# Optimization experiments

Hardware: AMD Instinct MI355X
Metric: run time of the kernel (lower is better)

The kernel has to match this reference:

```python
import jax, jax.numpy as jnp
import numpy as np

N = 50000


def gcn_conv(x, W, b, src, dst, deg_inv_sqrt):
    # h = x @ W, then symmetric-normalized aggregation with self-loops
    h = x @ W  # [N, out]
    norm = deg_inv_sqrt[src] * deg_inv_sqrt[dst]  # [E]
    agg = jax.ops.segment_sum(h[src] * norm[:, None], dst, num_segments=N)
    # self-loop contribution: norm_ii = deg_inv_sqrt[i]^2
    agg = agg + h * (deg_inv_sqrt * deg_inv_sqrt)[:, None]
    return agg + b


def setup_inputs() -> dict:
    key = jax.random.key(0)
    ks = jax.random.split(key, 8)
    F_in, H, C = 128, 128, 64
    x = jax.random.normal(ks[0], (N, F_in), dtype=jnp.float32)
    edge_index = jax.random.randint(ks[1], (2, 800000), 0, N, dtype=jnp.int64)
    s = 1.0 / np.sqrt(F_in)
    W1 = jax.random.uniform(ks[2], (F_in, H), jnp.float32, -s, s)
    b1 = jnp.zeros((H,), jnp.float32)
    W2 = jax.random.uniform(ks[3], (H, H), jnp.float32, -s, s)
    b2 = jnp.zeros((H,), jnp.float32)
    W3 = jax.random.uniform(ks[4], (H, C), jnp.float32, -s, s)
    b3 = jnp.zeros((C,), jnp.float32)
    return {"x": x, "edge_index": edge_index, "W1": W1, "b1": b1,
            "W2": W2, "b2": b2, "W3": W3, "b3": b3}


def reference(x, edge_index, W1, b1, W2, b2, W3, b3):
    src, dst = edge_index[0], edge_index[1]
    # degree with self-loops (edge weight 1): deg[i] = in-degree + 1
    deg = jnp.zeros((N,), x.dtype).at[dst].add(1.0) + 1.0
    dinv = jax.lax.rsqrt(deg)
    h = gcn_conv(x, W1, b1, src, dst, dinv)
    h = jax.nn.relu(h)  # dropout p=0 / eval -> identity
    h = gcn_conv(h, W2, b2, src, dst, dinv)
    h = jax.nn.relu(h)
    h = gcn_conv(h, W3, b3, src, dst, dinv)
    return jax.nn.log_softmax(h, axis=-1)
```

## Files before the change

kernel.cpp:

```cpp
#include <hip/hip_runtime.h>
#include <math.h>

typedef short short8 __attribute__((ext_vector_type(8)));
typedef float floatx4 __attribute__((ext_vector_type(4)));

__device__ __forceinline__ float4 ld4(const float* p) { return *reinterpret_cast<const float4*>(p); }
__device__ __forceinline__ void st4(float* p, float4 v) { *reinterpret_cast<float4*>(p) = v; }

__device__ __forceinline__ float bf2f(unsigned int u) { return __uint_as_float(u << 16); }
__device__ __forceinline__ unsigned int f2bf1(float f) {
    unsigned int x = __float_as_uint(f);
    return (x + 0x7fffu + ((x >> 16) & 1u)) >> 16;
}
__device__ __forceinline__ unsigned int f2bf2(float lo, float hi) {
    return f2bf1(lo) | (f2bf1(hi) << 16);
}
__device__ __forceinline__ void unpack8(uint4 v, float* f) {
    f[0] = bf2f(v.x & 0xffffu); f[1] = bf2f(v.x >> 16);
    f[2] = bf2f(v.y & 0xffffu); f[3] = bf2f(v.y >> 16);
    f[4] = bf2f(v.z & 0xffffu); f[5] = bf2f(v.z >> 16);
    f[6] = bf2f(v.w & 0xffffu); f[7] = bf2f(v.w >> 16);
}

__global__ __launch_bounds__(256) void k_count(const int* __restrict__ dst, int* __restrict__ deg, int E) {
    int e = blockIdx.x * 256 + threadIdx.x;
    if (e < E) atomicAdd(&deg[dst[e]], 1);
}

__global__ __launch_bounds__(256) void k_dinv(const int* __restrict__ deg, float* __restrict__ dinv, int n) {
    int i = blockIdx.x * 256 + threadIdx.x;
    if (i < n) dinv[i] = 1.0f / sqrtf((float)deg[i] + 1.0f);
}

__global__ __launch_bounds__(256) void k_reduce256(const int* __restrict__ deg, int* __restrict__ bsum, int n) {
    __shared__ int s[256];
    int t = threadIdx.x;
    int i = blockIdx.x * 256 + t;
    s[t] = (i < n) ? deg[i] : 0;
    __syncthreads();
    for (int off = 128; off > 0; off >>= 1) {
        if (t < off) s[t] += s[t + off];
        __syncthreads();
    }
    if (t == 0) bsum[blockIdx.x] = s[0];
}

__global__ __launch_bounds__(256) void k_scan_small(const int* __restrict__ bsum, int* __restrict__ boff, int nb) {
    __shared__ int s[256];
    int t = threadIdx.x;
    int v = (t < nb) ? bsum[t] : 0;
    s[t] = v;
    __syncthreads();
    for (int off = 1; off < 256; off <<= 1) {
        int x = (t >= off) ? s[t - off] : 0;
        __syncthreads();
        s[t] += x;
        __syncthreads();
    }
    if (t < nb) boff[t] = s[t] - v;
}

__global__ __launch_bounds__(256) void k_scan_final(const int* __restrict__ deg, const int* __restrict__ boff,
                                                    int* __restrict__ row_off, int* __restrict__ cursor, int n) {
    __shared__ int s[256];
    int t = threadIdx.x;
    int i = blockIdx.x * 256 + t;
    int v = (i < n) ? deg[i] : 0;
    s[t] = v;
    __syncthreads();
    for (int off = 1; off < 256; off <<= 1) {
        int x = (t >= off) ? s[t - off] : 0;
        __syncthreads();
        s[t] += x;
        __syncthreads();
    }
    int incl = s[t] + boff[blockIdx.x];
    if (i < n) {
        int ex = incl - v;
        row_off[i] = ex;
        cursor[i]  = ex;
        if (i == n - 1) row_off[n] = incl;
    }
}

__global__ __launch_bounds__(256) void k_fill(const int* __restrict__ src, const int* __restrict__ dst,
                                              const float* __restrict__ dinv, int* __restrict__ cursor,
                                              int2* __restrict__ cpair, int E) {
    int e = blockIdx.x * 256 + threadIdx.x;
    if (e < E) {
        int s = src[e], d = dst[e];
        int pos = atomicAdd(&cursor[d], 1);
        cpair[pos] = make_int2(s, __float_as_int(dinv[s] * dinv[d]));
    }
}

__global__ __launch_bounds__(256) void k_prepW(const float* __restrict__ W, unsigned short* __restrict__ Wt, int NC) {
    int t = blockIdx.x * 256 + threadIdx.x;
    if (t < NC * 128) {
        int k = t & 127, n = t >> 7;
        Wt[n * 128 + k] = (unsigned short)f2bf1(W[(size_t)k * NC + n]);
    }
}

template <int NC, bool XF32>
__global__ __launch_bounds__(256) void k_gemm_mfma(const void* __restrict__ Xv, const unsigned short* __restrict__ Wt,
                                                   unsigned short* __restrict__ O, int nrows) {
    constexpr int LDR = 136;
    __shared__ unsigned short sX[64 * LDR];
    __shared__ unsigned short sB[NC * LDR];

    const int tid  = threadIdx.x;
    const int row0 = blockIdx.x * 64;

    if constexpr (XF32) {
        const float* X = (const float*)Xv;
#pragma unroll
        for (int i = 0; i < 4; ++i) {
            int idx = tid + i * 256;
            int r = idx >> 4, c8 = idx & 15;
            int grow = row0 + r;
            uint4 v = make_uint4(0, 0, 0, 0);
            if (grow < nrows) {
                float4 a = ld4(X + (size_t)grow * 128 + c8 * 8);
                float4 b = ld4(X + (size_t)grow * 128 + c8 * 8 + 4);
                v = make_uint4(f2bf2(a.x, a.y), f2bf2(a.z, a.w), f2bf2(b.x, b.y), f2bf2(b.z, b.w));
            }
            *reinterpret_cast<uint4*>(&sX[r * LDR + c8 * 8]) = v;
        }
    } else {
        const unsigned short* X = (const unsigned short*)Xv;
#pragma unroll
        for (int i = 0; i < 4; ++i) {
            int idx = tid + i * 256;
            int r = idx >> 4, c8 = idx & 15;
            int grow = row0 + r;
            uint4 v = make_uint4(0, 0, 0, 0);
            if (grow < nrows) v = *reinterpret_cast<const uint4*>(X + (size_t)grow * 128 + c8 * 8);
            *reinterpret_cast<uint4*>(&sX[r * LDR + c8 * 8]) = v;
        }
    }
#pragma unroll
    for (int i = 0; i < NC / 16; ++i) {
        int idx = tid + i * 256;
        int n = idx >> 4, c8 = idx & 15;
        *reinterpret_cast<uint4*>(&sB[n * LDR + c8 * 8]) =
            *reinterpret_cast<const uint4*>(Wt + (size_t)n * 128 + c8 * 8);
    }
    __syncthreads();

    const int lane = tid & 63;
    const int wave = tid >> 6;
    const int l15  = lane & 15;
    const int quad = lane >> 4;

    floatx4 acc[NC / 16];
#pragma unroll
    for (int j = 0; j < NC / 16; ++j) acc[j] = (floatx4){0.f, 0.f, 0.f, 0.f};

    const unsigned short* xbase = &sX[(wave * 16 + l15) * LDR + quad * 8];
#pragma unroll
    for (int kk = 0; kk < 4; ++kk) {
        short8 xb = *reinterpret_cast<const short8*>(xbase + kk * 32);
#pragma unroll
        for (int j = 0; j < NC / 16; ++j) {
            short8 wa = *reinterpret_cast<const short8*>(&sB[(j * 16 + l15) * LDR + quad * 8 + kk * 32]);
            acc[j] = __builtin_amdgcn_mfma_f32_16x16x32_bf16(wa, xb, acc[j], 0, 0, 0);
        }
    }

    int xrow = row0 + wave * 16 + l15;
    if (xrow < nrows) {
#pragma unroll
        for (int j = 0; j < NC / 16; ++j) {
            uint2 o = make_uint2(f2bf2(acc[j][0], acc[j][1]), f2bf2(acc[j][2], acc[j][3]));
            *reinterpret_cast<uint2*>(O + (size_t)xrow * NC + j * 16 + quad * 4) = o;
        }
    }
}

__global__ __launch_bounds__(256) void k_agg_relu(const unsigned short* __restrict__ H, const int* __restrict__ roff,
                                                  const int2* __restrict__ cpair, const float* __restrict__ dinv,
                                                  const float* __restrict__ bias, unsigned short* __restrict__ O, int n) {
    int t    = blockIdx.x * 256 + threadIdx.x;
    int node = t >> 4;
    int f8   = (t & 15) * 8;
    if (node >= n) return;

    float di = dinv[node];
    float sc = di * di;
    float a[8];
    {
        uint4 hv = *reinterpret_cast<const uint4*>(H + (size_t)node * 128 + f8);
        float h[8];
        unpack8(hv, h);
#pragma unroll
        for (int i = 0; i < 8; ++i) a[i] = h[i] * sc;
    }

    int e  = roff[node];
    int e1 = roff[node + 1];
    for (; e + 1 < e1; e += 2) {
        int2 p0 = cpair[e], p1 = cpair[e + 1];
        float n0 = __int_as_float(p0.y), n1 = __int_as_float(p1.y);
        uint4 v0 = *reinterpret_cast<const uint4*>(H + (size_t)p0.x * 128 + f8);
        uint4 v1 = *reinterpret_cast<const uint4*>(H + (size_t)p1.x * 128 + f8);
        float g0[8], g1[8];
        unpack8(v0, g0);
        unpack8(v1, g1);
#pragma unroll
        for (int i = 0; i < 8; ++i) a[i] += g0[i] * n0 + g1[i] * n1;
    }
    if (e < e1) {
        int2 p0 = cpair[e];
        float n0 = __int_as_float(p0.y);
        uint4 v0 = *reinterpret_cast<const uint4*>(H + (size_t)p0.x * 128 + f8);
        float g0[8];
        unpack8(v0, g0);
#pragma unroll
        for (int i = 0; i < 8; ++i) a[i] += g0[i] * n0;
    }

    float4 b0 = ld4(bias + f8);
    float4 b1 = ld4(bias + f8 + 4);
    float bb[8] = {b0.x, b0.y, b0.z, b0.w, b1.x, b1.y, b1.z, b1.w};
#pragma unroll
    for (int i = 0; i < 8; ++i) a[i] = fmaxf(a[i] + bb[i], 0.0f);

    uint4 ov = make_uint4(f2bf2(a[0], a[1]), f2bf2(a[2], a[3]), f2bf2(a[4], a[5]), f2bf2(a[6], a[7]));
    *reinterpret_cast<uint4*>(O + (size_t)node * 128 + f8) = ov;
}

__global__ __launch_bounds__(256) void k_agg_softmax(const unsigned short* __restrict__ H, const int* __restrict__ roff,
                                                     const int2* __restrict__ cpair, const float* __restrict__ dinv,
                                                     const float* __restrict__ bias, float* __restrict__ O, int n) {
    int t    = blockIdx.x * 256 + threadIdx.x;
    int node = t >> 3;
    int f8   = (t & 7) * 8;
    if (node >= n) return;

    float di = dinv[node];
    float sc = di * di;
    float a[8];
    {
        uint4 hv = *reinterpret_cast<const uint4*>(H + (size_t)node * 64 + f8);
        float h[8];
        unpack8(hv, h);
#pragma unroll
        for (int i = 0; i < 8; ++i) a[i] = h[i] * sc;
    }

    int e  = roff[node];
    int e1 = roff[node + 1];
    for (; e + 1 < e1; e += 2) {
        int2 p0 = cpair[e], p1 = cpair[e + 1];
        float n0 = __int_as_float(p0.y), n1 = __int_as_float(p1.y);
        uint4 v0 = *reinterpret_cast<const uint4*>(H + (size_t)p0.x * 64 + f8);
        uint4 v1 = *reinterpret_cast<const uint4*>(H + (size_t)p1.x * 64 + f8);
        float g0[8], g1[8];
        unpack8(v0, g0);
        unpack8(v1, g1);
#pragma unroll
        for (int i = 0; i < 8; ++i) a[i] += g0[i] * n0 + g1[i] * n1;
    }
    if (e < e1) {
        int2 p0 = cpair[e];
        float n0 = __int_as_float(p0.y);
        uint4 v0 = *reinterpret_cast<const uint4*>(H + (size_t)p0.x * 64 + f8);
        float g0[8];
        unpack8(v0, g0);
#pragma unroll
        for (int i = 0; i < 8; ++i) a[i] += g0[i] * n0;
    }

    float4 b0 = ld4(bias + f8);
    float4 b1 = ld4(bias + f8 + 4);
    float bb[8] = {b0.x, b0.y, b0.z, b0.w, b1.x, b1.y, b1.z, b1.w};
    float v[8];
#pragma unroll
    for (int i = 0; i < 8; ++i) v[i] = a[i] + bb[i];

    float m = v[0];
#pragma unroll
    for (int i = 1; i < 8; ++i) m = fmaxf(m, v[i]);
    m = fmaxf(m, __shfl_xor(m, 1));
    m = fmaxf(m, __shfl_xor(m, 2));
    m = fmaxf(m, __shfl_xor(m, 4));

    float ssum = 0.0f;
#pragma unroll
    for (int i = 0; i < 8; ++i) ssum += expf(v[i] - m);
    ssum += __shfl_xor(ssum, 1);
    ssum += __shfl_xor(ssum, 2);
    ssum += __shfl_xor(ssum, 4);
    float ls = logf(ssum);

    float* op = O + (size_t)node * 64 + f8;
    st4(op, make_float4(v[0] - m - ls, v[1] - m - ls, v[2] - m - ls, v[3] - m - ls));
    st4(op + 4, make_float4(v[4] - m - ls, v[5] - m - ls, v[6] - m - ls, v[7] - m - ls));
}

extern "C" void kernel_launch(void* const* d_in, const int* in_sizes, int n_in,
                              void* d_out, int out_size, void* d_ws, size_t ws_size,
                              hipStream_t stream) {
    const float* x  = (const float*)d_in[0];
    const int*   ei = (const int*)d_in[1];
    const float* W1 = (const float*)d_in[2];
    const float* b1 = (const float*)d_in[3];
    const float* W2 = (const float*)d_in[4];
    const float* b2 = (const float*)d_in[5];
    const float* W3 = (const float*)d_in[6];
    const float* b3 = (const float*)d_in[7];
    float* out = (float*)d_out;

    const int N = in_sizes[0] / 128;
    const int E = in_sizes[1] / 2;
    const int* src = ei;
    const int* dst = ei + E;

    char* ws = (char*)d_ws;
    size_t off = 0;
    auto alloc = [&](size_t bytes) -> char* {
        char* p = ws + off;
        off = (off + bytes + 255) & ~(size_t)255;
        return p;
    };
    int nb = (N + 255) / 256;
    int*   deg     = (int*)alloc((size_t)N * 4);
    int*   cursor  = (int*)alloc((size_t)N * 4);
    int*   row_off = (int*)alloc(((size_t)N + 1) * 4);
    float* dinv    = (float*)alloc((size_t)N * 4);
    int*   bsum    = (int*)alloc((size_t)nb * 4);
    int*   boff    = (int*)alloc((size_t)nb * 4);
    int2*  cpair   = (int2*)alloc((size_t)E * 8);
    unsigned short* Wt1  = (unsigned short*)alloc(128 * 128 * 2);
    unsigned short* Wt2  = (unsigned short*)alloc(128 * 128 * 2);
    unsigned short* Wt3  = (unsigned short*)alloc(64 * 128 * 2);
    unsigned short* bufA = (unsigned short*)alloc((size_t)N * 128 * 2);
    unsigned short* bufB = (unsigned short*)alloc((size_t)N * 128 * 2);
    unsigned short* bufC = (unsigned short*)alloc((size_t)N * 64 * 2);
    (void)ws_size; (void)n_in; (void)out_size;

    hipMemsetAsync(deg, 0, (size_t)N * 4, stream);
    k_count<<<(E + 255) / 256, 256, 0, stream>>>(dst, deg, E);
    k_dinv<<<(N + 255) / 256, 256, 0, stream>>>(deg, dinv, N);
    k_reduce256<<<nb, 256, 0, stream>>>(deg, bsum, N);
    k_scan_small<<<1, 256, 0, stream>>>(bsum, boff, nb);
    k_scan_final<<<nb, 256, 0, stream>>>(deg, boff, row_off, cursor, N);
    k_fill<<<(E + 255) / 256, 256, 0, stream>>>(src, dst, dinv, cursor, cpair, E);

    k_prepW<<<(128 * 128 + 255) / 256, 256, 0, stream>>>(W1, Wt1, 128);
    k_prepW<<<(128 * 128 + 255) / 256, 256, 0, stream>>>(W2, Wt2, 128);
    k_prepW<<<(64 * 128 + 255) / 256, 256, 0, stream>>>(W3, Wt3, 64);

    int gemm_blocks = (N + 63) / 64;
    k_gemm_mfma<128, true><<<gemm_blocks, 256, 0, stream>>>(x, Wt1, bufA, N);
    k_agg_relu<<<((size_t)N * 16 + 255) / 256, 256, 0, stream>>>(bufA, row_off, cpair, dinv, b1, bufB, N);
    k_gemm_mfma<128, false><<<gemm_blocks, 256, 0, stream>>>(bufB, Wt2, bufA, N);
    k_agg_relu<<<((size_t)N * 16 + 255) / 256, 256, 0, stream>>>(bufA, row_off, cpair, dinv, b2, bufB, N);
    k_gemm_mfma<64, false><<<gemm_blocks, 256, 0, stream>>>(bufB, Wt3, bufC, N);
    k_agg_softmax<<<((size_t)N * 8 + 255) / 256, 256, 0, stream>>>(bufC, row_off, cpair, dinv, b3, out, N);
}
```

Before: 291.8 us.

## Record edge ranks during counting, fuse dinv and prepW launches, unroll gathers by four

The degree-count kernel now stores each edge's atomic return value as its rank, so the CSR fill computes positions as row_off plus rank instead of issuing a second pass of atomics on a cursor array. The dinv computation is folded into the final scan kernel, and the three weight-conversion launches are merged into one. The aggregation loops are unrolled by four, loading all four edge pairs and their gathered rows before accumulating to expose more memory-level parallelism. The trade-off is an extra E-sized rank array that is written and then read back, plus somewhat higher register pressure in the aggregation kernels.

After: 257.7 us. 11.7% less time.

```diff
diff --git a/kernel.cpp b/kernel.cpp
--- a/kernel.cpp
+++ b/kernel.cpp
@@ -22,14 +22,10 @@
     f[6] = bf2f(v.w & 0xffffu); f[7] = bf2f(v.w >> 16);
 }
 
-__global__ __launch_bounds__(256) void k_count(const int* __restrict__ dst, int* __restrict__ deg, int E) {
+__global__ __launch_bounds__(256) void k_count(const int* __restrict__ dst, int* __restrict__ deg,
+                                               int* __restrict__ rank, int E) {
     int e = blockIdx.x * 256 + threadIdx.x;
-    if (e < E) atomicAdd(&deg[dst[e]], 1);
-}
-
-__global__ __launch_bounds__(256) void k_dinv(const int* __restrict__ deg, float* __restrict__ dinv, int n) {
-    int i = blockIdx.x * 256 + threadIdx.x;
-    if (i < n) dinv[i] = 1.0f / sqrtf((float)deg[i] + 1.0f);
+    if (e < E) rank[e] = atomicAdd(&deg[dst[e]], 1);
 }
 
 __global__ __launch_bounds__(256) void k_reduce256(const int* __restrict__ deg, int* __restrict__ bsum, int n) {
@@ -61,7 +57,7 @@
 }
 
 __global__ __launch_bounds__(256) void k_scan_final(const int* __restrict__ deg, const int* __restrict__ boff,
-                                                    int* __restrict__ row_off, int* __restrict__ cursor, int n) {
+                                                    int* __restrict__ row_off, float* __restrict__ dinv, int n) {
     __shared__ int s[256];
     int t = threadIdx.x;
     int i = blockIdx.x * 256 + t;
@@ -76,29 +72,38 @@
     }
     int incl = s[t] + boff[blockIdx.x];
     if (i < n) {
-        int ex = incl - v;
-        row_off[i] = ex;
-        cursor[i]  = ex;
+        row_off[i] = incl - v;
+        dinv[i]    = 1.0f / sqrtf((float)v + 1.0f);
         if (i == n - 1) row_off[n] = incl;
     }
 }
 
 __global__ __launch_bounds__(256) void k_fill(const int* __restrict__ src, const int* __restrict__ dst,
-                                              const float* __restrict__ dinv, int* __restrict__ cursor,
-                                              int2* __restrict__ cpair, int E) {
+                                              const int* __restrict__ rank, const int* __restrict__ roff,
+                                              const float* __restrict__ dinv, int2* __restrict__ cpair, int E) {
     int e = blockIdx.x * 256 + threadIdx.x;
     if (e < E) {
         int s = src[e], d = dst[e];
-        int pos = atomicAdd(&cursor[d], 1);
+        int pos = roff[d] + rank[e];
         cpair[pos] = make_int2(s, __float_as_int(dinv[s] * dinv[d]));
     }
 }
 
-__global__ __launch_bounds__(256) void k_prepW(const float* __restrict__ W, unsigned short* __restrict__ Wt, int NC) {
+__global__ __launch_bounds__(256) void k_prepW(const float* __restrict__ W1, const float* __restrict__ W2,
+                                               const float* __restrict__ W3, unsigned short* __restrict__ Wt1,
+                                               unsigned short* __restrict__ Wt2, unsigned short* __restrict__ Wt3) {
     int t = blockIdx.x * 256 + threadIdx.x;
-    if (t < NC * 128) {
+    if (t < 16384) {
         int k = t & 127, n = t >> 7;
-        Wt[n * 128 + k] = (unsigned short)f2bf1(W[(size_t)k * NC + n]);
+        Wt1[n * 128 + k] = (unsigned short)f2bf1(W1[(size_t)k * 128 + n]);
+    } else if (t < 32768) {
+        int u = t - 16384;
+        int k = u & 127, n = u >> 7;
+        Wt2[n * 128 + k] = (unsigned short)f2bf1(W2[(size_t)k * 128 + n]);
+    } else if (t < 40960) {
+        int u = t - 32768;
+        int k = u & 127, n = u >> 7;
+        Wt3[n * 128 + k] = (unsigned short)f2bf1(W3[(size_t)k * 64 + n]);
     }
 }
 
@@ -199,18 +204,23 @@
 
     int e  = roff[node];
     int e1 = roff[node + 1];
-    for (; e + 1 < e1; e += 2) {
-        int2 p0 = cpair[e], p1 = cpair[e + 1];
-        float n0 = __int_as_float(p0.y), n1 = __int_as_float(p1.y);
-        uint4 v0 = *reinterpret_cast<const uint4*>(H + (size_t)p0.x * 128 + f8);
-        uint4 v1 = *reinterpret_cast<const uint4*>(H + (size_t)p1.x * 128 + f8);
-        float g0[8], g1[8];
-        unpack8(v0, g0);
-        unpack8(v1, g1);
-#pragma unroll
-        for (int i = 0; i < 8; ++i) a[i] += g0[i] * n0 + g1[i] * n1;
-    }
-    if (e < e1) {
+    for (; e + 3 < e1; e += 4) {
+        int2 p[4];
+        uint4 v[4];
+#pragma unroll
+        for (int u = 0; u < 4; ++u) p[u] = cpair[e + u];
+#pragma unroll
+        for (int u = 0; u < 4; ++u) v[u] = *reinterpret_cast<const uint4*>(H + (size_t)p[u].x * 128 + f8);
+#pragma unroll
+        for (int u = 0; u < 4; ++u) {
+            float nu = __int_as_float(p[u].y);
+            float g[8];
+            unpack8(v[u], g);
+#pragma unroll
+            for (int i = 0; i < 8; ++i) a[i] += g[i] * nu;
+        }
+    }
+    for (; e < e1; ++e) {
         int2 p0 = cpair[e];
         float n0 = __int_as_float(p0.y);
         uint4 v0 = *reinterpret_cast<const uint4*>(H + (size_t)p0.x * 128 + f8);
@@ -251,18 +261,23 @@
 
     int e  = roff[node];
     int e1 = roff[node + 1];
-    for (; e + 1 < e1; e += 2) {
-        int2 p0 = cpair[e], p1 = cpair[e + 1];
-        float n0 = __int_as_float(p0.y), n1 = __int_as_float(p1.y);
-        uint4 v0 = *reinterpret_cast<const uint4*>(H + (size_t)p0.x * 64 + f8);
-        uint4 v1 = *reinterpret_cast<const uint4*>(H + (size_t)p1.x * 64 + f8);
-        float g0[8], g1[8];
-        unpack8(v0, g0);
-        unpack8(v1, g1);
-#pragma unroll
-        for (int i = 0; i < 8; ++i) a[i] += g0[i] * n0 + g1[i] * n1;
-    }
-    if (e < e1) {
+    for (; e + 3 < e1; e += 4) {
+        int2 p[4];
+        uint4 v[4];
+#pragma unroll
+        for (int u = 0; u < 4; ++u) p[u] = cpair[e + u];
+#pragma unroll
+        for (int u = 0; u < 4; ++u) v[u] = *reinterpret_cast<const uint4*>(H + (size_t)p[u].x * 64 + f8);
+#pragma unroll
+        for (int u = 0; u < 4; ++u) {
+            float nu = __int_as_float(p[u].y);
+            float g[8];
+            unpack8(v[u], g);
+#pragma unroll
+            for (int i = 0; i < 8; ++i) a[i] += g[i] * nu;
+        }
+    }
+    for (; e < e1; ++e) {
         int2 p0 = cpair[e];
         float n0 = __int_as_float(p0.y);
         uint4 v0 = *reinterpret_cast<const uint4*>(H + (size_t)p0.x * 64 + f8);
@@ -326,11 +341,11 @@
     };
     int nb = (N + 255) / 256;
     int*   deg     = (int*)alloc((size_t)N * 4);
-    int*   cursor  = (int*)alloc((size_t)N * 4);
     int*   row_off = (int*)alloc(((size_t)N + 1) * 4);
     float* dinv    = (float*)alloc((size_t)N * 4);
     int*   bsum    = (int*)alloc((size_t)nb * 4);
     int*   boff    = (int*)alloc((size_t)nb * 4);
+    int*   rank    = (int*)alloc((size_t)E * 4);
     int2*  cpair   = (int2*)alloc((size_t)E * 8);
     unsigned short* Wt1  = (unsigned short*)alloc(128 * 128 * 2);
     unsigned short* Wt2  = (unsigned short*)alloc(128 * 128 * 2);
@@ -341,16 +356,13 @@
     (void)ws_size; (void)n_in; (void)out_size;
 
     hipMemsetAsync(deg, 0, (size_t)N * 4, stream);
-    k_count<<<(E + 255) / 256, 256, 0, stream>>>(dst, deg, E);
-    k_dinv<<<(N + 255) / 256, 256, 0, stream>>>(deg, dinv, N);
+    k_count<<<(E + 255) / 256, 256, 0, stream>>>(dst, deg, rank, E);
     k_reduce256<<<nb, 256, 0, stream>>>(deg, bsum, N);
     k_scan_small<<<1, 256, 0, stream>>>(bsum, boff, nb);
-    k_scan_final<<<nb, 256, 0, stream>>>(deg, boff, row_off, cursor, N);
-    k_fill<<<(E + 255) / 256, 256, 0, stream>>>(src, dst, dinv, cursor, cpair, E);
-
-    k_prepW<<<(128 * 128 + 255) / 256, 256, 0, stream>>>(W1, Wt1, 128);
-    k_prepW<<<(128 * 128 + 255) / 256, 256, 0, stream>>>(W2, Wt2, 128);
-    k_prepW<<<(64 * 128 + 255) / 256, 256, 0, stream>>>(W3, Wt3, 64);
+    k_scan_final<<<nb, 256, 0, stream>>>(deg, boff, row_off, dinv, N);
+    k_fill<<<(E + 255) / 256, 256, 0, stream>>>(src, dst, rank, row_off, dinv, cpair, E);
+
+    k_prepW<<<(40960 + 255) / 256, 256, 0, stream>>>(W1, W2, W3, Wt1, Wt2, Wt3);
 
     int gemm_blocks = (N + 63) / 64;
     k_gemm_mfma<128, true><<<gemm_blocks, 256, 0, stream>>>(x, Wt1, bufA, N);
```
